# Optimization experiments

Measured on AMD Instinct MI355X. Metric: run time of the kernel, lower is better.

The kernel has to match this reference:

```python
import jax, jax.numpy as jnp
import numpy as np

H = 8        # attention heads
G = 8        # groupnorm groups
EPS = 1e-5

def mish(x):
    return x * jnp.tanh(jnp.logaddexp(x, 0.0))

def conv1d(x, w, b, pad):
    # x: [B,C,L], w: [O,I,K]
    y = jax.lax.conv_general_dilated(x, w, (1,), [(pad, pad)],
                                     dimension_numbers=('NCH', 'OIH', 'NCH'))
    return y + b[None, :, None]

def gn_per_step(x, gamma, beta):
    # torch code reshapes [B,C,L] -> [(B L), C] and applies GroupNorm(G, C):
    # normalize each (b, l) position over channel groups.
    B, C, L = x.shape
    xg = x.reshape(B, G, C // G, L)
    mean = xg.mean(axis=2, keepdims=True)
    var = xg.var(axis=2, keepdims=True)
    xg = (xg - mean) * jax.lax.rsqrt(var + EPS)
    return xg.reshape(B, C, L) * gamma[None, :, None] + beta[None, :, None]

def layernorm(x, g, b):
    mean = x.mean(axis=-1, keepdims=True)
    var = x.var(axis=-1, keepdims=True)
    return (x - mean) * jax.lax.rsqrt(var + EPS) * g + b


def setup_inputs() -> dict:
    key = jax.random.key(0)
    ks = jax.random.split(key, 16)
    B, Cin, Cout, L, N, CD, TD = 64, 256, 512, 512, 77, 768, 512
    w = lambda k, shape, s=0.02: (jax.random.normal(k, shape, jnp.float32) * s)
    return {
        'x': jax.random.normal(ks[0], (B, Cin, L), jnp.float32),
        't': jax.random.normal(ks[1], (B, TD), jnp.float32),
        'cond': jax.random.normal(ks[2], (B, N, CD), jnp.float32),
        'conv0_w': w(ks[3], (Cout, Cin, 5)), 'conv0_b': jnp.zeros((Cout,), jnp.float32),
        'gn0_g': jnp.ones((Cout,), jnp.float32), 'gn0_b': jnp.zeros((Cout,), jnp.float32),
        'tm_w': w(ks[4], (2 * Cout, TD)), 'tm_b': jnp.zeros((2 * Cout,), jnp.float32),
        'conv1_w': w(ks[5], (Cout, Cout, 5)), 'conv1_b': jnp.zeros((Cout,), jnp.float32),
        'gn1_g': jnp.ones((Cout,), jnp.float32), 'gn1_b': jnp.zeros((Cout,), jnp.float32),
        'res_w': w(ks[6], (Cout, Cin, 1)), 'res_b': jnp.zeros((Cout,), jnp.float32),
        'ln_x_g': jnp.ones((Cout,), jnp.float32), 'ln_x_b': jnp.zeros((Cout,), jnp.float32),
        'ln_c_g': jnp.ones((CD,), jnp.float32), 'ln_c_b': jnp.zeros((CD,), jnp.float32),
        'q_w': w(ks[7], (Cout, Cout)), 'q_b': jnp.zeros((Cout,), jnp.float32),
        'k_w': w(ks[8], (Cout, CD)), 'k_b': jnp.zeros((Cout,), jnp.float32),
        'v_w': w(ks[9], (Cout, CD)), 'v_b': jnp.zeros((Cout,), jnp.float32),
        'cond_indices': jnp.arange(B, dtype=jnp.int64 if jax.config.jax_enable_x64 else jnp.int32),
    }


def _forward(x, t, cond,
             conv0_w, conv0_b, gn0_g, gn0_b, tm_w, tm_b,
             conv1_w, conv1_b, gn1_g, gn1_b, res_w, res_b,
             ln_x_g, ln_x_b, ln_c_g, ln_c_b,
             q_w, q_b, k_w, k_b, v_w, v_b, cond_indices):
    Cout = conv0_w.shape[0]
    # ---- ResidualTemporalBlock (adagn=True) ----
    ss = jnp.einsum('bi,oi->bo', mish(t), tm_w) + tm_b        # [B, 2*Cout]
    scale = ss[:, :Cout, None]                                 # chunk dim=1
    shift = ss[:, Cout:, None]
    h = conv1d(x, conv0_w, conv0_b, pad=2)                     # [B,Cout,L]
    h = gn_per_step(h, gn0_g, gn0_b)
    h = mish(h * (1.0 + scale) + shift)                        # ada_shift_scale + Mish
    h = conv1d(h, conv1_w, conv1_b, pad=2)
    h = mish(gn_per_step(h, gn1_g, gn1_b))
    out = h + conv1d(x, res_w, res_b, pad=0)                   # residual 1x1 conv
    # ---- ResidualCrossAttentionLayer (LinearCrossAttention) ----
    xs = out[cond_indices]                                     # [Bc,Cout,L]
    xi = xs.transpose(0, 2, 1)                                 # [Bc,L,Cout]
    cs = cond[cond_indices]                                    # [Bc,N,CD]
    Bc, T, D = xi.shape
    Nn = cs.shape[1]
    Dh = D // H
    q = jnp.einsum('btl,dl->btd', layernorm(xi, ln_x_g, ln_x_b), q_w) + q_b
    cn = layernorm(cs, ln_c_g, ln_c_b)
    k = jnp.einsum('bnl,dl->bnd', cn, k_w) + k_b
    v = jnp.einsum('bnl,dl->bnd', cn, v_w) + v_b
    q = jax.nn.softmax(q.reshape(Bc, T, H, Dh), axis=-1)       # softmax over head dim
    k = jax.nn.softmax(k.reshape(Bc, Nn, H, Dh), axis=1)       # softmax over tokens
    v = v.reshape(Bc, Nn, H, Dh)
    attn = jnp.einsum('bnhd,bnhl->bhdl', k, v)                 # [Bc,H,Dh,Dh] kernel
    y = jnp.einsum('bthd,bhdl->bthl', q, attn).reshape(Bc, T, D)
    return out.at[cond_indices].add(y.transpose(0, 2, 1))


def reference(x, t, cond,
              conv0_w, conv0_b, gn0_g, gn0_b, tm_w, tm_b,
              conv1_w, conv1_b, gn1_g, gn1_b, res_w, res_b,
              ln_x_g, ln_x_b, ln_c_g, ln_c_b,
              q_w, q_b, k_w, k_b, v_w, v_b, cond_indices):
    return _forward(x, t, cond, conv0_w, conv0_b, gn0_g, gn0_b, tm_w, tm_b,
                    conv1_w, conv1_b, gn1_g, gn1_b, res_w, res_b,
                    ln_x_g, ln_x_b, ln_c_g, ln_c_b,
                    q_w, q_b, k_w, k_b, v_w, v_b, cond_indices)
```

## Files before the change

kernel.cpp:

```cpp
#include <hip/hip_runtime.h>
#include <math.h>

#define EPS 1e-5f

typedef __attribute__((ext_vector_type(8))) short short8;
typedef __attribute__((ext_vector_type(4))) float floatx4;

typedef __attribute__((address_space(1))) const void* gas1_t;
typedef __attribute__((address_space(3))) void* las3_t;

__device__ __forceinline__ void glls16(const void* g, void* l) {
    __builtin_amdgcn_global_load_lds((gas1_t)g, (las3_t)l, 16, 0, 0);
}

__device__ __forceinline__ float mishf(float x) {
    float sp = fmaxf(x, 0.0f) + log1pf(expf(-fabsf(x)));
    return x * tanhf(sp);
}
__device__ __forceinline__ unsigned short f2bf(float f) {
    unsigned int u = __float_as_uint(f);
    unsigned int r = (u + 0x7fffu + ((u >> 16) & 1u)) >> 16;
    return (unsigned short)r;
}
__device__ __forceinline__ float bf2f(unsigned short s) {
    return __uint_as_float(((unsigned int)s) << 16);
}
__device__ __forceinline__ unsigned int pk2(unsigned short a, unsigned short b) {
    return (unsigned int)a | ((unsigned int)b << 16);
}

__global__ __launch_bounds__(256) void setup_k(
        const float* __restrict__ conv0_w, const float* __restrict__ conv1_w,
        const float* __restrict__ res_w, const float* __restrict__ q_w,
        const float* __restrict__ k_w, const float* __restrict__ v_w,
        const float* __restrict__ t,
        unsigned short* __restrict__ wp0, unsigned short* __restrict__ wp1,
        unsigned short* __restrict__ wr, unsigned short* __restrict__ wq,
        unsigned short* __restrict__ wk, unsigned short* __restrict__ wvv,
        float* __restrict__ mt,
        unsigned short* __restrict__ xTp, unsigned short* __restrict__ h0Tp) {
    const int blk = blockIdx.x, tid = threadIdx.x;
    if (blk < 2560) {
        int o = blk * 256 + tid;
        int ci = o & 255, co = (o >> 8) & 511, kk = o >> 17;
        wp0[o] = f2bf(conv0_w[((size_t)co * 256 + ci) * 5 + kk]);
    } else if (blk < 7680) {
        int o = (blk - 2560) * 256 + tid;
        int ci = o & 511, co = (o >> 9) & 511, kk = o >> 18;
        wp1[o] = f2bf(conv1_w[((size_t)co * 512 + ci) * 5 + kk]);
    } else if (blk < 7808) {
        int i = (blk - 7680) * 256 + tid;
        float4 f = *(const float4*)&res_w[(size_t)i * 4];
        *(uint2*)&wr[(size_t)i * 4] =
            make_uint2(pk2(f2bf(f.x), f2bf(f.y)), pk2(f2bf(f.z), f2bf(f.w)));
    } else if (blk < 8064) {
        int i = (blk - 7808) * 256 + tid;
        float4 f = *(const float4*)&q_w[(size_t)i * 4];
        *(uint2*)&wq[(size_t)i * 4] =
            make_uint2(pk2(f2bf(f.x), f2bf(f.y)), pk2(f2bf(f.z), f2bf(f.w)));
    } else if (blk < 8448) {
        int i = (blk - 8064) * 256 + tid;
        float4 f = *(const float4*)&k_w[(size_t)i * 4];
        *(uint2*)&wk[(size_t)i * 4] =
            make_uint2(pk2(f2bf(f.x), f2bf(f.y)), pk2(f2bf(f.z), f2bf(f.w)));
    } else if (blk < 8832) {
        int i = (blk - 8448) * 256 + tid;
        float4 f = *(const float4*)&v_w[(size_t)i * 4];
        *(uint2*)&wvv[(size_t)i * 4] =
            make_uint2(pk2(f2bf(f.x), f2bf(f.y)), pk2(f2bf(f.z), f2bf(f.w)));
    } else if (blk < 8960) {
        int i = (blk - 8832) * 256 + tid;
        mt[i] = mishf(t[i]);
    } else if (blk < 8992) {
        int idx = (blk - 8960) * 256 + tid;
        int u = idx * 8;
        int c = u & 255, r4 = (u >> 8) & 3, b = u >> 10;
        int row = (r4 < 2) ? r4 : (512 + r4);
        *(uint4*)&xTp[((size_t)b * 516 + row) * 256 + c] = make_uint4(0, 0, 0, 0);
    } else {
        int idx = (blk - 8992) * 256 + tid;
        int u = idx * 8;
        int c = u & 511, r4 = (u >> 9) & 3, b = u >> 11;
        int row = (r4 < 2) ? r4 : (512 + r4);
        *(uint4*)&h0Tp[((size_t)b * 516 + row) * 512 + c] = make_uint4(0, 0, 0, 0);
    }
}

__global__ __launch_bounds__(256) void xpose_cvt(const float* __restrict__ x,
        unsigned short* __restrict__ xT) {
    __shared__ float tile[64][68];
    const int tid = threadIdx.x;
    const int l0 = blockIdx.x * 64, c0 = blockIdx.y * 64, b = blockIdx.z;
    for (int idx = tid; idx < 64 * 16; idx += 256) {
        int cr = idx >> 4, lc = (idx & 15) * 4;
        float4 f = *(const float4*)&x[((size_t)b * 256 + c0 + cr) * 512 + l0 + lc];
        tile[cr][lc] = f.x; tile[cr][lc + 1] = f.y;
        tile[cr][lc + 2] = f.z; tile[cr][lc + 3] = f.w;
    }
    __syncthreads();
    for (int idx = tid; idx < 64 * 16; idx += 256) {
        int lr = idx >> 4, cc = (idx & 15) * 4;
        *(uint2*)&xT[((size_t)b * 516 + 2 + l0 + lr) * 256 + c0 + cc] =
            make_uint2(pk2(f2bf(tile[cc][lr]), f2bf(tile[cc + 1][lr])),
                       pk2(f2bf(tile[cc + 2][lr]), f2bf(tile[cc + 3][lr])));
    }
}

template<int KD>
__global__ __launch_bounds__(256) void gemm_nt(const float* __restrict__ A,
        const float* __restrict__ W, const float* __restrict__ bias,
        float* __restrict__ C, int M, int N) {
    constexpr int ST = 20;
    __shared__ __align__(16) float As[64 * ST];
    __shared__ __align__(16) float Ws[64 * ST];
    const int tid = threadIdx.x;
    const int r0 = blockIdx.x * 64, c0 = blockIdx.y * 64;
    const int tx = tid & 15, ty = tid >> 4;
    const int lrow = tid >> 2, lk = (tid & 3) * 4;
    float acc[4][4];
#pragma unroll
    for (int i = 0; i < 4; ++i)
#pragma unroll
        for (int j = 0; j < 4; ++j) acc[i][j] = 0.f;
    for (int k0 = 0; k0 < KD; k0 += 16) {
        __syncthreads();
        *(float4*)&As[lrow * ST + lk] =
            *(const float4*)&A[(size_t)(r0 + lrow) * KD + k0 + lk];
        *(float4*)&Ws[lrow * ST + lk] =
            *(const float4*)&W[(size_t)(c0 + lrow) * KD + k0 + lk];
        __syncthreads();
#pragma unroll
        for (int kk = 0; kk < 16; kk += 4) {
            float4 av[4], wv[4];
#pragma unroll
            for (int i = 0; i < 4; ++i)
                av[i] = *(const float4*)&As[(ty + 16 * i) * ST + kk];
#pragma unroll
            for (int j = 0; j < 4; ++j)
                wv[j] = *(const float4*)&Ws[(tx + 16 * j) * ST + kk];
#pragma unroll
            for (int i = 0; i < 4; ++i)
#pragma unroll
                for (int j = 0; j < 4; ++j) {
                    acc[i][j] = fmaf(av[i].x, wv[j].x, acc[i][j]);
                    acc[i][j] = fmaf(av[i].y, wv[j].y, acc[i][j]);
                    acc[i][j] = fmaf(av[i].z, wv[j].z, acc[i][j]);
                    acc[i][j] = fmaf(av[i].w, wv[j].w, acc[i][j]);
                }
        }
    }
#pragma unroll
    for (int j = 0; j < 4; ++j) {
        int c = c0 + tx + 16 * j;
        float bv = bias[c];
#pragma unroll
        for (int i = 0; i < 4; ++i)
            C[(size_t)(r0 + ty + 16 * i) * N + c] = acc[i][j] + bv;
    }
}

template<int CI, bool FILM, bool OPAD>
__global__ __launch_bounds__(256) void conv5_mfma(
        const unsigned short* __restrict__ xb,
        const unsigned short* __restrict__ wp,
        const float* __restrict__ bias,
        const float* __restrict__ gam, const float* __restrict__ bet,
        const float* __restrict__ ss,
        unsigned short* __restrict__ outT) {
    constexpr int NC = CI / 32;
    __shared__ __align__(16) unsigned short xs[2][260 * 32];
    __shared__ __align__(16) unsigned short wsm[2][5 * 64 * 32];
    __shared__ float sgam[64], sbet[64], sbias[64], sscale[64], sshift[64];

    const int tid = threadIdx.x;
    const int l0 = blockIdx.x * 256;
    const int co0 = blockIdx.y * 64;
    const int b = blockIdx.z;
    const int lane = tid & 63;
    const int wv = tid >> 6;
    const int lq = lane & 15, qd = lane >> 4;
    const int wn = wv * 64;

    if (tid < 64) {
        int co = co0 + tid;
        sbias[tid] = bias[co];
        sgam[tid] = gam[co];
        sbet[tid] = bet[co];
        if (FILM) {
            sscale[tid] = ss[(size_t)b * 1024 + co];
            sshift[tid] = ss[(size_t)b * 1024 + 512 + co];
        }
    }

    const unsigned short* gxb = xb + ((size_t)b * 516 + l0) * CI;
    const unsigned short* gwb = wp + (size_t)co0 * CI;

    const unsigned short* xsp[5];
    const unsigned short* wsp[5];
    unsigned sdo[5];
#pragma unroll
    for (int it = 0; it < 5; ++it) {
        int task = it * 256 + tid;
        {
            int ri = task >> 2, pos = task & 3;
            int seg = pos ^ ((ri >> 1) & 3);
            xsp[it] = gxb + (size_t)ri * CI + seg * 8;
        }
        {
            int kk = task >> 8, r = task & 255;
            int col = r >> 2, pos = r & 3;
            int seg = pos ^ ((col >> 1) & 3);
            wsp[it] = gwb + ((size_t)kk * 512 + col) * CI + seg * 8;
        }
        sdo[it] = (unsigned)(it * 256 + wn) * 8;
    }
    const bool xv4 = tid < 16;

    auto stage = [&](int buf) {
#pragma unroll
        for (int it = 0; it < 5; ++it) {
            if (it < 4 || xv4) glls16(xsp[it], &xs[buf][sdo[it]]);
            xsp[it] += 32;
        }
#pragma unroll
        for (int it = 0; it < 5; ++it) {
            glls16(wsp[it], &wsm[buf][sdo[it]]);
            wsp[it] += 32;
        }
    };

    unsigned bvo[5][4], avo[5][4];
#pragma unroll
    for (int kk = 0; kk < 5; ++kk) {
#pragma unroll
        for (int j = 0; j < 4; ++j) {
            int row = wn + j * 16 + lq + kk;
            int pos = qd ^ ((row >> 1) & 3);
            bvo[kk][j] = (unsigned)(row * 32 + pos * 8) * 2u;
        }
#pragma unroll
        for (int i = 0; i < 4; ++i) {
            int crow = i * 16 + lq;
            int pos = qd ^ ((crow >> 1) & 3);
            avo[kk][i] = (unsigned)(kk * 2048 + crow * 32 + pos * 8) * 2u;
        }
    }

    floatx4 acc[4][4];
#pragma unroll
    for (int i = 0; i < 4; ++i)
#pragma unroll
        for (int j = 0; j < 4; ++j) acc[i][j] = (floatx4){0.f, 0.f, 0.f, 0.f};

    auto compute = [&](int buf) {
        const char* xr = (const char*)xs[buf];
        const char* wr_ = (const char*)wsm[buf];
#pragma unroll
        for (int kk = 0; kk < 5; ++kk) {
            short8 bvf[4];
#pragma unroll
            for (int j = 0; j < 4; ++j)
                bvf[j] = *(const short8*)(xr + bvo[kk][j]);
#pragma unroll
            for (int i = 0; i < 4; ++i) {
                short8 av = *(const short8*)(wr_ + avo[kk][i]);
#pragma unroll
                for (int j = 0; j < 4; ++j)
                    acc[i][j] = __builtin_amdgcn_mfma_f32_16x16x32_bf16(
                        av, bvf[j], acc[i][j], 0, 0, 0);
            }
        }
    };

    stage(0);
    stage(1);
    __syncthreads();
#pragma unroll 1
    for (int c = 0; c < NC; ++c) {
        __builtin_amdgcn_s_setprio(1);
        compute(c & 1);
        __builtin_amdgcn_s_setprio(0);
        if (c + 1 < NC) {
            __builtin_amdgcn_s_barrier();
            if (c + 2 < NC) {
                stage(c & 1);
                asm volatile("s_waitcnt vmcnt(9)" ::: "memory");
            } else {
                asm volatile("s_waitcnt vmcnt(0)" ::: "memory");
            }
            __builtin_amdgcn_s_barrier();
        }
    }

    float m_[4], rs_[4];
#pragma unroll
    for (int j = 0; j < 4; ++j) {
        float s1 = 0.f, s2 = 0.f;
#pragma unroll
        for (int i = 0; i < 4; ++i) {
            float4 bv4 = *(const float4*)&sbias[i * 16 + qd * 4];
            float ba[4] = {bv4.x, bv4.y, bv4.z, bv4.w};
#pragma unroll
            for (int r = 0; r < 4; ++r) {
                float v = acc[i][j][r] + ba[r];
                acc[i][j][r] = v;
                s1 += v; s2 += v * v;
            }
        }
        s1 += __shfl_xor(s1, 16, 64); s2 += __shfl_xor(s2, 16, 64);
        s1 += __shfl_xor(s1, 32, 64); s2 += __shfl_xor(s2, 32, 64);
        float mean = s1 * (1.f / 64.f);
        float var = s2 * (1.f / 64.f) - mean * mean;
        m_[j] = mean; rs_[j] = rsqrtf(var + EPS);
    }
#pragma unroll
    for (int j = 0; j < 4; ++j) {
        int l = l0 + wn + j * 16 + lq;
        size_t rowbase = OPAD ? (((size_t)b * 516 + 2 + l) * 512 + co0)
                              : (((size_t)b * 512 + l) * 512 + co0);
#pragma unroll
        for (int i = 0; i < 4; ++i) {
            float4 g4 = *(const float4*)&sgam[i * 16 + qd * 4];
            float4 b4 = *(const float4*)&sbet[i * 16 + qd * 4];
            float ga[4] = {g4.x, g4.y, g4.z, g4.w};
            float be[4] = {b4.x, b4.y, b4.z, b4.w};
            float sa[4] = {0, 0, 0, 0}, sh[4] = {0, 0, 0, 0};
            if (FILM) {
                float4 s4 = *(const float4*)&sscale[i * 16 + qd * 4];
                float4 h4 = *(const float4*)&sshift[i * 16 + qd * 4];
                sa[0] = s4.x; sa[1] = s4.y; sa[2] = s4.z; sa[3] = s4.w;
                sh[0] = h4.x; sh[1] = h4.y; sh[2] = h4.z; sh[3] = h4.w;
            }
            unsigned short o[4];
#pragma unroll
            for (int r = 0; r < 4; ++r) {
                float v = (acc[i][j][r] - m_[j]) * rs_[j] * ga[r] + be[r];
                if (FILM) v = v * (1.f + sa[r]) + sh[r];
                o[r] = f2bf(mishf(v));
            }
            *(uint2*)&outT[rowbase + i * 16 + qd * 4] =
                make_uint2(pk2(o[0], o[1]), pk2(o[2], o[3]));
        }
    }
}

template<int KD, int EPI, bool PADA>
__global__ __launch_bounds__(256) void gemm1_mfma(
        const unsigned short* __restrict__ A,
        const unsigned short* __restrict__ W,
        const float* __restrict__ bias,
        const unsigned short* __restrict__ addT,
        float* __restrict__ outF,
        unsigned short* __restrict__ outB,
        int Mreal) {
    constexpr int NC = KD / 32;
    __shared__ __align__(16) unsigned short xs[2][256 * 32];
    __shared__ __align__(16) unsigned short wsm[2][64 * 32];
    __shared__ float sbias[64];
    const int tid = threadIdx.x;
    const int m0 = blockIdx.x * 256;
    const int n0 = blockIdx.y * 64;
    const int lane = tid & 63;
    const int wv = tid >> 6;
    const int lq = lane & 15, qd = lane >> 4;
    const int wn = wv * 64;
    if (tid < 64) sbias[tid] = bias[n0 + tid];

    const size_t arow0 = PADA ? ((size_t)(m0 >> 9) * 516 + 2 + (m0 & 511))
                              : (size_t)m0;
    const unsigned short* gA = A + arow0 * KD;
    const unsigned short* gW = W + (size_t)n0 * KD;

    const unsigned short* xp[4];
#pragma unroll
    for (int it = 0; it < 4; ++it) {
        int task = it * 256 + tid;
        int ri = task >> 2, pos = task & 3;
        int seg = pos ^ ((ri >> 1) & 3);
        xp[it] = gA + (size_t)ri * KD + seg * 8;
    }
    const unsigned short* wpq;
    {
        int col = tid >> 2, pos = tid & 3;
        int seg = pos ^ ((col >> 1) & 3);
        wpq = gW + (size_t)col * KD + seg * 8;
    }

    auto stage = [&](int buf) {
#pragma unroll
        for (int it = 0; it < 4; ++it) {
            glls16(xp[it], &xs[buf][(unsigned)(it * 256 + wn) * 8]);
            xp[it] += 32;
        }
        glls16(wpq, &wsm[buf][(unsigned)wn * 8]);
        wpq += 32;
    };

    unsigned bvo[4], avo[4];
#pragma unroll
    for (int j = 0; j < 4; ++j) {
        int row = wn + j * 16 + lq;
        int pos = qd ^ ((row >> 1) & 3);
        bvo[j] = (unsigned)(row * 32 + pos * 8) * 2u;
    }
#pragma unroll
    for (int i = 0; i < 4; ++i) {
        int crow = i * 16 + lq;
        int pos = qd ^ ((crow >> 1) & 3);
        avo[i] = (unsigned)(crow * 32 + pos * 8) * 2u;
    }

    floatx4 acc[4][4];
#pragma unroll
    for (int i = 0; i < 4; ++i)
#pragma unroll
        for (int j = 0; j < 4; ++j) acc[i][j] = (floatx4){0.f, 0.f, 0.f, 0.f};

    auto compute = [&](int buf) {
        const char* xr = (const char*)xs[buf];
        const char* wr_ = (const char*)wsm[buf];
        short8 bvf[4];
#pragma unroll
        for (int j = 0; j < 4; ++j)
            bvf[j] = *(const short8*)(xr + bvo[j]);
#pragma unroll
        for (int i = 0; i < 4; ++i) {
            short8 av = *(const short8*)(wr_ + avo[i]);
#pragma unroll
            for (int j = 0; j < 4; ++j)
                acc[i][j] = __builtin_amdgcn_mfma_f32_16x16x32_bf16(
                    av, bvf[j], acc[i][j], 0, 0, 0);
        }
    };

    stage(0);
    stage(1);
    __syncthreads();
#pragma unroll 1
    for (int c = 0; c < NC; ++c) {
        __builtin_amdgcn_s_setprio(1);
        compute(c & 1);
        __builtin_amdgcn_s_setprio(0);
        if (c + 1 < NC) {
            __builtin_amdgcn_s_barrier();
            if (c + 2 < NC) {
                stage(c & 1);
                asm volatile("s_waitcnt vmcnt(5)" ::: "memory");
            } else {
                asm volatile("s_waitcnt vmcnt(0)" ::: "memory");
            }
            __builtin_amdgcn_s_barrier();
        }
    }

#pragma unroll
    for (int i = 0; i < 4; ++i) {
        float4 bv4 = *(const float4*)&sbias[i * 16 + qd * 4];
        float ba[4] = {bv4.x, bv4.y, bv4.z, bv4.w};
#pragma unroll
        for (int j = 0; j < 4; ++j)
#pragma unroll
            for (int r = 0; r < 4; ++r) acc[i][j][r] += ba[r];
    }
    if (EPI == 0) {
#pragma unroll
        for (int j = 0; j < 4; ++j) {
            int m = m0 + wn + j * 16 + lq;
#pragma unroll
            for (int i = 0; i < 4; ++i) {
                int n = n0 + i * 16 + qd * 4;
                uint2 hv = *(const uint2*)&addT[(size_t)m * 512 + n];
                float vr[4];
                vr[0] = acc[i][j][0] + bf2f((unsigned short)(hv.x & 0xffff));
                vr[1] = acc[i][j][1] + bf2f((unsigned short)(hv.x >> 16));
                vr[2] = acc[i][j][2] + bf2f((unsigned short)(hv.y & 0xffff));
                vr[3] = acc[i][j][3] + bf2f((unsigned short)(hv.y >> 16));
                *(uint2*)&outB[(size_t)m * 512 + n] =
                    make_uint2(pk2(f2bf(vr[0]), f2bf(vr[1])),
                               pk2(f2bf(vr[2]), f2bf(vr[3])));
            }
        }
    } else if (EPI == 1) {
#pragma unroll
        for (int j = 0; j < 4; ++j) {
            float mx = -3.4e38f;
#pragma unroll
            for (int i = 0; i < 4; ++i)
#pragma unroll
                for (int r = 0; r < 4; ++r) mx = fmaxf(mx, acc[i][j][r]);
            mx = fmaxf(mx, __shfl_xor(mx, 16, 64));
            mx = fmaxf(mx, __shfl_xor(mx, 32, 64));
            float s = 0.f;
#pragma unroll
            for (int i = 0; i < 4; ++i)
#pragma unroll
                for (int r = 0; r < 4; ++r) {
                    float e = expf(acc[i][j][r] - mx);
                    acc[i][j][r] = e; s += e;
                }
            s += __shfl_xor(s, 16, 64);
            s += __shfl_xor(s, 32, 64);
            float inv = 1.f / s;
            int m = m0 + wn + j * 16 + lq;
#pragma unroll
            for (int i = 0; i < 4; ++i) {
                *(uint2*)&outB[(size_t)m * 512 + n0 + i * 16 + qd * 4] =
                    make_uint2(pk2(f2bf(acc[i][j][0] * inv), f2bf(acc[i][j][1] * inv)),
                               pk2(f2bf(acc[i][j][2] * inv), f2bf(acc[i][j][3] * inv)));
            }
        }
    } else {
#pragma unroll
        for (int j = 0; j < 4; ++j) {
            int m = m0 + wn + j * 16 + lq;
            if (m < Mreal) {
#pragma unroll
                for (int i = 0; i < 4; ++i) {
                    float4 o = {acc[i][j][0], acc[i][j][1], acc[i][j][2], acc[i][j][3]};
                    *(float4*)&outF[(size_t)m * 512 + n0 + i * 16 + qd * 4] = o;
                }
            }
        }
    }
}

__global__ __launch_bounds__(256) void lnrow(const unsigned short* __restrict__ src,
        const float* __restrict__ g, const float* __restrict__ be,
        const int* __restrict__ cidx, unsigned short* __restrict__ dst) {
    const int tid = threadIdx.x;
    const int lane = tid & 63, wv = tid >> 6;
    const int row0 = blockIdx.x * 32 + wv * 8;
    for (int rr = 0; rr < 8; ++rr) {
        int m = row0 + rr;
        int b = m >> 9, t = m & 511;
        int ib = cidx[b];
        const unsigned short* sp = &src[((size_t)ib * 512 + t) * 512 + lane * 8];
        short8 u = *(const short8*)sp;
        float v[8];
        float s1 = 0.f, s2 = 0.f;
#pragma unroll
        for (int k = 0; k < 8; ++k) {
            v[k] = bf2f(((const unsigned short*)&u)[k]);
            s1 += v[k]; s2 += v[k] * v[k];
        }
#pragma unroll
        for (int o = 32; o > 0; o >>= 1) {
            s1 += __shfl_xor(s1, o, 64);
            s2 += __shfl_xor(s2, o, 64);
        }
        float mean = s1 * (1.f / 512.f);
        float var = s2 * (1.f / 512.f) - mean * mean;
        float rs = rsqrtf(var + EPS);
        float4 g0 = *(const float4*)&g[lane * 8];
        float4 g1 = *(const float4*)&g[lane * 8 + 4];
        float4 b0 = *(const float4*)&be[lane * 8];
        float4 b1 = *(const float4*)&be[lane * 8 + 4];
        float ga[8] = {g0.x, g0.y, g0.z, g0.w, g1.x, g1.y, g1.z, g1.w};
        float ba[8] = {b0.x, b0.y, b0.z, b0.w, b1.x, b1.y, b1.z, b1.w};
        unsigned short o8[8];
#pragma unroll
        for (int k = 0; k < 8; ++k)
            o8[k] = f2bf((v[k] - mean) * rs * ga[k] + ba[k]);
        *(uint4*)&dst[(size_t)m * 512 + lane * 8] =
            make_uint4(pk2(o8[0], o8[1]), pk2(o8[2], o8[3]),
                       pk2(o8[4], o8[5]), pk2(o8[6], o8[7]));
    }
}

__global__ __launch_bounds__(256) void lnc_k(const float* __restrict__ cond,
        const float* __restrict__ g, const float* __restrict__ be,
        const int* __restrict__ cidx, unsigned short* __restrict__ cn) {
    const int tid = threadIdx.x;
    const int bn = blockIdx.x;
    const int b = bn / 77, n = bn - b * 77;
    const int ib = cidx[b];
    const float* src = cond + ((size_t)ib * 77 + n) * 768;
    float v[3];
    float s = 0.f, s2 = 0.f;
#pragma unroll
    for (int i = 0; i < 3; ++i) {
        v[i] = src[tid + i * 256];
        s += v[i]; s2 += v[i] * v[i];
    }
#pragma unroll
    for (int o = 32; o > 0; o >>= 1) {
        s += __shfl_xor(s, o, 64);
        s2 += __shfl_xor(s2, o, 64);
    }
    __shared__ float r1[4], r2[4], mv[2];
    if ((tid & 63) == 0) { r1[tid >> 6] = s; r2[tid >> 6] = s2; }
    __syncthreads();
    if (tid == 0) {
        float ts = r1[0] + r1[1] + r1[2] + r1[3];
        float ts2 = r2[0] + r2[1] + r2[2] + r2[3];
        float m = ts * (1.f / 768.f);
        float var = ts2 * (1.f / 768.f) - m * m;
        mv[0] = m; mv[1] = rsqrtf(var + EPS);
    }
    __syncthreads();
    float m = mv[0], rs = mv[1];
    unsigned short* dst = cn + ((size_t)b * 77 + n) * 768;
#pragma unroll
    for (int i = 0; i < 3; ++i) {
        int c = tid + i * 256;
        dst[c] = f2bf((v[i] - m) * rs * g[c] + be[c]);
    }
}

__global__ __launch_bounds__(256) void attn_k(const float* __restrict__ k,
        const float* __restrict__ v, unsigned short* __restrict__ attnT) {
    constexpr int NS = 68;
    __shared__ __align__(16) float ks[77 * NS];
    __shared__ __align__(16) float vs[77 * NS];
    __shared__ float red[2][256];
    const int tid = threadIdx.x;
    const int b = blockIdx.x >> 3, h = blockIdx.x & 7;
    for (int idx = tid; idx < 77 * 16; idx += 256) {
        int n = idx >> 4, dq2 = (idx & 15) * 4;
        *(float4*)&ks[n * NS + dq2] =
            *(const float4*)&k[((size_t)b * 77 + n) * 512 + h * 64 + dq2];
        *(float4*)&vs[n * NS + dq2] =
            *(const float4*)&v[((size_t)b * 77 + n) * 512 + h * 64 + dq2];
    }
    __syncthreads();
    {
        const int d = tid & 63, grp = tid >> 6;
        float mx = -3.4e38f;
        for (int n = grp; n < 77; n += 4) mx = fmaxf(mx, ks[n * NS + d]);
        red[0][grp * 64 + d] = mx;
        __syncthreads();
        mx = fmaxf(fmaxf(red[0][d], red[0][64 + d]),
                   fmaxf(red[0][128 + d], red[0][192 + d]));
        float s = 0.f;
        for (int n = grp; n < 77; n += 4) {
            float e = expf(ks[n * NS + d] - mx);
            ks[n * NS + d] = e; s += e;
        }
        red[1][grp * 64 + d] = s;
        __syncthreads();
        float inv = 1.f / (red[1][d] + red[1][64 + d] + red[1][128 + d] + red[1][192 + d]);
        for (int n = grp; n < 77; n += 4) ks[n * NS + d] *= inv;
    }
    __syncthreads();
    const int e = tid & 63, dq = tid >> 6;
    float acc[16];
#pragma unroll
    for (int u = 0; u < 16; ++u) acc[u] = 0.f;
    for (int n = 0; n < 77; ++n) {
        float vv = vs[n * NS + e];
#pragma unroll
        for (int u4 = 0; u4 < 4; ++u4) {
            float4 kk = *(const float4*)&ks[n * NS + dq * 16 + u4 * 4];
            acc[u4 * 4 + 0] = fmaf(kk.x, vv, acc[u4 * 4 + 0]);
            acc[u4 * 4 + 1] = fmaf(kk.y, vv, acc[u4 * 4 + 1]);
            acc[u4 * 4 + 2] = fmaf(kk.z, vv, acc[u4 * 4 + 2]);
            acc[u4 * 4 + 3] = fmaf(kk.w, vv, acc[u4 * 4 + 3]);
        }
    }
    unsigned short ob[16];
#pragma unroll
    for (int u = 0; u < 16; ++u) ob[u] = f2bf(acc[u]);
    size_t base = (((size_t)b * 8 + h) * 64 + e) * 64 + dq * 16;
    *(uint4*)&attnT[base] = make_uint4(pk2(ob[0], ob[1]), pk2(ob[2], ob[3]),
                                       pk2(ob[4], ob[5]), pk2(ob[6], ob[7]));
    *(uint4*)&attnT[base + 8] = make_uint4(pk2(ob[8], ob[9]), pk2(ob[10], ob[11]),
                                           pk2(ob[12], ob[13]), pk2(ob[14], ob[15]));
}

__global__ __launch_bounds__(256) void yattn_final(
        const unsigned short* __restrict__ q,
        const unsigned short* __restrict__ at,
        const unsigned short* __restrict__ resT,
        const int* __restrict__ cidx, float* __restrict__ out) {
    const int tid = threadIdx.x;
    const int lane = tid & 63, wv = tid >> 6;
    const int lq = lane & 15, qd = lane >> 4;
    const int t0 = blockIdx.x * 256 + wv * 64;
    const int h = blockIdx.y, b = blockIdx.z;
    const int ib = cidx[b];
    floatx4 acc[4][4];
#pragma unroll
    for (int i = 0; i < 4; ++i)
#pragma unroll
        for (int j = 0; j < 4; ++j) acc[i][j] = (floatx4){0.f, 0.f, 0.f, 0.f};
#pragma unroll
    for (int ks = 0; ks < 2; ++ks) {
        short8 av[4], bv[4];
#pragma unroll
        for (int i = 0; i < 4; ++i)
            av[i] = *(const short8*)
                &q[((size_t)(b * 512 + t0 + i * 16 + lq)) * 512 + h * 64 + ks * 32 + qd * 8];
#pragma unroll
        for (int j = 0; j < 4; ++j)
            bv[j] = *(const short8*)
                &at[(((size_t)(b * 8 + h)) * 64 + j * 16 + lq) * 64 + ks * 32 + qd * 8];
#pragma unroll
        for (int i = 0; i < 4; ++i)
#pragma unroll
            for (int j = 0; j < 4; ++j)
                acc[i][j] = __builtin_amdgcn_mfma_f32_16x16x32_bf16(
                    av[i], bv[j], acc[i][j], 0, 0, 0);
    }
#pragma unroll
    for (int j = 0; j < 4; ++j) {
        int c = h * 64 + j * 16 + lq;
#pragma unroll
        for (int i = 0; i < 4; ++i) {
            int tb = t0 + i * 16 + qd * 4;
            float vr[4];
#pragma unroll
            for (int r = 0; r < 4; ++r)
                vr[r] = acc[i][j][r] +
                        bf2f(resT[((size_t)(ib * 512 + tb + r)) * 512 + c]);
            float4 o = {vr[0], vr[1], vr[2], vr[3]};
            *(float4*)&out[((size_t)ib * 512 + c) * 512 + tb] = o;
        }
    }
}

extern "C" void kernel_launch(void* const* d_in, const int* in_sizes, int n_in,
                              void* d_out, int out_size, void* d_ws, size_t ws_size,
                              hipStream_t stream) {
    (void)in_sizes; (void)n_in; (void)out_size; (void)ws_size;
    const float* x       = (const float*)d_in[0];
    const float* t       = (const float*)d_in[1];
    const float* cond    = (const float*)d_in[2];
    const float* conv0_w = (const float*)d_in[3];
    const float* conv0_b = (const float*)d_in[4];
    const float* gn0_g   = (const float*)d_in[5];
    const float* gn0_b   = (const float*)d_in[6];
    const float* tm_w    = (const float*)d_in[7];
    const float* tm_b    = (const float*)d_in[8];
    const float* conv1_w = (const float*)d_in[9];
    const float* conv1_b = (const float*)d_in[10];
    const float* gn1_g   = (const float*)d_in[11];
    const float* gn1_b   = (const float*)d_in[12];
    const float* res_w   = (const float*)d_in[13];
    const float* res_b   = (const float*)d_in[14];
    const float* ln_x_g  = (const float*)d_in[15];
    const float* ln_x_b  = (const float*)d_in[16];
    const float* ln_c_g  = (const float*)d_in[17];
    const float* ln_c_b  = (const float*)d_in[18];
    const float* q_w     = (const float*)d_in[19];
    const float* q_b     = (const float*)d_in[20];
    const float* k_w     = (const float*)d_in[21];
    const float* k_b     = (const float*)d_in[22];
    const float* v_w     = (const float*)d_in[23];
    const float* v_b     = (const float*)d_in[24];
    const int*   cidx    = (const int*)d_in[25];
    float* out = (float*)d_out;

    char* WS = (char*)d_ws;
    unsigned short* xTp   = (unsigned short*)(WS + 0);
    unsigned short* cnb   = (unsigned short*)(WS + 0);
    unsigned short* attnT = (unsigned short*)(WS + 8388608);
    unsigned short* h0Tp  = (unsigned short*)(WS + 16908288);
    unsigned short* xlnT  = (unsigned short*)(WS + 16908288);
    float*          kb    = (float*)(WS + 16908288);
    float*          vb    = (float*)(WS + 27000832);
    unsigned short* h1T   = (unsigned short*)(WS + 50724864);
    unsigned short* qbf   = (unsigned short*)(WS + 50724864);
    unsigned short* outTb = (unsigned short*)(WS + 84279296);
    unsigned short* wp0   = (unsigned short*)(WS + 117833728);
    unsigned short* wp1   = (unsigned short*)(WS + 119144448);
    unsigned short* wr    = (unsigned short*)(WS + 121765888);
    unsigned short* wq    = (unsigned short*)(WS + 122028032);
    unsigned short* wk    = (unsigned short*)(WS + 122552320);
    unsigned short* wvv   = (unsigned short*)(WS + 123338752);
    float*          ssb   = (float*)(WS + 124125184);
    float*          mt    = (float*)(WS + 124387328);

    setup_k<<<dim3(9056), dim3(256), 0, stream>>>(
        conv0_w, conv1_w, res_w, q_w, k_w, v_w, t,
        wp0, wp1, wr, wq, wk, wvv, mt, xTp, h0Tp);
    xpose_cvt<<<dim3(8, 4, 64), dim3(256), 0, stream>>>(x, xTp);
    gemm_nt<512><<<dim3(1, 16), dim3(256), 0, stream>>>(mt, tm_w, tm_b, ssb, 64, 1024);
    conv5_mfma<256, true, true><<<dim3(2, 8, 64), dim3(256), 0, stream>>>(
        xTp, wp0, conv0_b, gn0_g, gn0_b, ssb, h0Tp);
    conv5_mfma<512, false, false><<<dim3(2, 8, 64), dim3(256), 0, stream>>>(
        h0Tp, wp1, conv1_b, gn1_g, gn1_b, (const float*)nullptr, h1T);
    gemm1_mfma<256, 0, true><<<dim3(128, 8), dim3(256), 0, stream>>>(
        xTp, wr, res_b, h1T, (float*)nullptr, outTb, 32768);
    lnrow<<<dim3(1024), dim3(256), 0, stream>>>(outTb, ln_x_g, ln_x_b, cidx, xlnT);
    gemm1_mfma<512, 1, false><<<dim3(128, 8), dim3(256), 0, stream>>>(
        xlnT, wq, q_b, (const unsigned short*)nullptr, (float*)nullptr, qbf, 32768);
    lnc_k<<<dim3(4928), dim3(256), 0, stream>>>(cond, ln_c_g, ln_c_b, cidx, cnb);
    gemm1_mfma<768, 2, false><<<dim3(20, 8), dim3(256), 0, stream>>>(
        cnb, wk, k_b, (const unsigned short*)nullptr, kb, (unsigned short*)nullptr, 4928);
    gemm1_mfma<768, 2, false><<<dim3(20, 8), dim3(256), 0, stream>>>(
        cnb, wvv, v_b, (const unsigned short*)nullptr, vb, (unsigned short*)nullptr, 4928);
    attn_k<<<dim3(512), dim3(256), 0, stream>>>(kb, vb, attnT);
    yattn_final<<<dim3(2, 8, 64), dim3(256), 0, stream>>>(qbf, attnT, outTb, cidx, out);
}
```

Before: 620.9 us.

## Single-buffer weight tiles via register staging to cut LDS and raise occupancy

In the conv5 and gemm1 MFMA kernels, weight tiles are no longer double-buffered in LDS. They are prefetched into registers two chunks ahead and written into a single LDS buffer between barriers. Per-channel bias, gamma, beta and FiLM parameters in conv5 are read straight from global memory instead of being staged in shared memory. Launch bounds now request 3 or 4 blocks per CU. The goal is lower LDS use so more blocks fit per CU, at the cost of extra registers, manual vmcnt bookkeeping and a synchronous LDS store on the critical path each iteration.

```diff
diff --git a/kernel.cpp b/kernel.cpp
--- a/kernel.cpp
+++ b/kernel.cpp
@@ -160,7 +160,7 @@
 }
 
 template<int CI, bool FILM, bool OPAD>
-__global__ __launch_bounds__(256) void conv5_mfma(
+__global__ __launch_bounds__(256, 3) void conv5_mfma(
         const unsigned short* __restrict__ xb,
         const unsigned short* __restrict__ wp,
         const float* __restrict__ bias,
@@ -169,8 +169,7 @@
         unsigned short* __restrict__ outT) {
     constexpr int NC = CI / 32;
     __shared__ __align__(16) unsigned short xs[2][260 * 32];
-    __shared__ __align__(16) unsigned short wsm[2][5 * 64 * 32];
-    __shared__ float sgam[64], sbet[64], sbias[64], sscale[64], sshift[64];
+    __shared__ __align__(16) unsigned short wsm[5 * 64 * 32];
 
     const int tid = threadIdx.x;
     const int l0 = blockIdx.x * 256;
@@ -181,22 +180,11 @@
     const int lq = lane & 15, qd = lane >> 4;
     const int wn = wv * 64;
 
-    if (tid < 64) {
-        int co = co0 + tid;
-        sbias[tid] = bias[co];
-        sgam[tid] = gam[co];
-        sbet[tid] = bet[co];
-        if (FILM) {
-            sscale[tid] = ss[(size_t)b * 1024 + co];
-            sshift[tid] = ss[(size_t)b * 1024 + 512 + co];
-        }
-    }
-
     const unsigned short* gxb = xb + ((size_t)b * 516 + l0) * CI;
     const unsigned short* gwb = wp + (size_t)co0 * CI;
 
     const unsigned short* xsp[5];
-    const unsigned short* wsp[5];
+    const unsigned short* wbp[5];
     unsigned sdo[5];
 #pragma unroll
     for (int it = 0; it < 5; ++it) {
@@ -210,23 +198,30 @@
             int kk = task >> 8, r = task & 255;
             int col = r >> 2, pos = r & 3;
             int seg = pos ^ ((col >> 1) & 3);
-            wsp[it] = gwb + ((size_t)kk * 512 + col) * CI + seg * 8;
+            wbp[it] = gwb + ((size_t)kk * 512 + col) * CI + seg * 8;
         }
         sdo[it] = (unsigned)(it * 256 + wn) * 8;
     }
     const bool xv4 = tid < 16;
 
-    auto stage = [&](int buf) {
+    auto stageX = [&](int buf) {
 #pragma unroll
         for (int it = 0; it < 5; ++it) {
             if (it < 4 || xv4) glls16(xsp[it], &xs[buf][sdo[it]]);
             xsp[it] += 32;
         }
-#pragma unroll
-        for (int it = 0; it < 5; ++it) {
-            glls16(wsp[it], &wsm[buf][sdo[it]]);
-            wsp[it] += 32;
-        }
+    };
+
+    uint4 wreg[5];
+    auto wload = [&](int c) {
+#pragma unroll
+        for (int it = 0; it < 5; ++it)
+            wreg[it] = *(const uint4*)(wbp[it] + (size_t)c * 32);
+    };
+    auto wstore = [&]() {
+#pragma unroll
+        for (int it = 0; it < 5; ++it)
+            *(uint4*)((char*)wsm + (unsigned)(it * 256 + tid) * 16u) = wreg[it];
     };
 
     unsigned bvo[5][4], avo[5][4];
@@ -254,7 +249,7 @@
 
     auto compute = [&](int buf) {
         const char* xr = (const char*)xs[buf];
-        const char* wr_ = (const char*)wsm[buf];
+        const char* wr_ = (const char*)wsm;
 #pragma unroll
         for (int kk = 0; kk < 5; ++kk) {
             short8 bvf[4];
@@ -272,9 +267,13 @@
         }
     };
 
-    stage(0);
-    stage(1);
+    stageX(0);
+#pragma unroll
+    for (int it = 0; it < 5; ++it) glls16(wbp[it], &wsm[sdo[it]]);
+    stageX(1);
+    wload(1);
     __syncthreads();
+
 #pragma unroll 1
     for (int c = 0; c < NC; ++c) {
         __builtin_amdgcn_s_setprio(1);
@@ -282,23 +281,31 @@
         __builtin_amdgcn_s_setprio(0);
         if (c + 1 < NC) {
             __builtin_amdgcn_s_barrier();
+            asm volatile("s_waitcnt vmcnt(9)" ::: "memory");
+            wstore();
             if (c + 2 < NC) {
-                stage(c & 1);
-                asm volatile("s_waitcnt vmcnt(9)" ::: "memory");
+                wload(c + 2);
+                stageX(c & 1);
+                asm volatile("s_waitcnt vmcnt(14)" ::: "memory");
             } else {
                 asm volatile("s_waitcnt vmcnt(0)" ::: "memory");
             }
+            asm volatile("s_waitcnt lgkmcnt(0)" ::: "memory");
             __builtin_amdgcn_s_barrier();
         }
     }
 
+    const float* bb = bias + co0;
+    const float* gb = gam + co0;
+    const float* eb = bet + co0;
+    const float* sb = FILM ? (ss + (size_t)b * 1024 + co0) : nullptr;
     float m_[4], rs_[4];
 #pragma unroll
     for (int j = 0; j < 4; ++j) {
         float s1 = 0.f, s2 = 0.f;
 #pragma unroll
         for (int i = 0; i < 4; ++i) {
-            float4 bv4 = *(const float4*)&sbias[i * 16 + qd * 4];
+            float4 bv4 = *(const float4*)&bb[i * 16 + qd * 4];
             float ba[4] = {bv4.x, bv4.y, bv4.z, bv4.w};
 #pragma unroll
             for (int r = 0; r < 4; ++r) {
@@ -320,14 +327,14 @@
                               : (((size_t)b * 512 + l) * 512 + co0);
 #pragma unroll
         for (int i = 0; i < 4; ++i) {
-            float4 g4 = *(const float4*)&sgam[i * 16 + qd * 4];
-            float4 b4 = *(const float4*)&sbet[i * 16 + qd * 4];
+            float4 g4 = *(const float4*)&gb[i * 16 + qd * 4];
+            float4 b4 = *(const float4*)&eb[i * 16 + qd * 4];
             float ga[4] = {g4.x, g4.y, g4.z, g4.w};
             float be[4] = {b4.x, b4.y, b4.z, b4.w};
             float sa[4] = {0, 0, 0, 0}, sh[4] = {0, 0, 0, 0};
             if (FILM) {
-                float4 s4 = *(const float4*)&sscale[i * 16 + qd * 4];
-                float4 h4 = *(const float4*)&sshift[i * 16 + qd * 4];
+                float4 s4 = *(const float4*)&sb[i * 16 + qd * 4];
+                float4 h4 = *(const float4*)&sb[512 + i * 16 + qd * 4];
                 sa[0] = s4.x; sa[1] = s4.y; sa[2] = s4.z; sa[3] = s4.w;
                 sh[0] = h4.x; sh[1] = h4.y; sh[2] = h4.z; sh[3] = h4.w;
             }
@@ -345,7 +352,7 @@
 }
 
 template<int KD, int EPI, bool PADA>
-__global__ __launch_bounds__(256) void gemm1_mfma(
+__global__ __launch_bounds__(256, 4) void gemm1_mfma(
         const unsigned short* __restrict__ A,
         const unsigned short* __restrict__ W,
         const float* __restrict__ bias,
@@ -355,7 +362,7 @@
         int Mreal) {
     constexpr int NC = KD / 32;
     __shared__ __align__(16) unsigned short xs[2][256 * 32];
-    __shared__ __align__(16) unsigned short wsm[2][64 * 32];
+    __shared__ __align__(16) unsigned short wsm[64 * 32];
     __shared__ float sbias[64];
     const int tid = threadIdx.x;
     const int m0 = blockIdx.x * 256;
@@ -379,21 +386,25 @@
         int seg = pos ^ ((ri >> 1) & 3);
         xp[it] = gA + (size_t)ri * KD + seg * 8;
     }
-    const unsigned short* wpq;
+    const unsigned short* wbp;
     {
         int col = tid >> 2, pos = tid & 3;
         int seg = pos ^ ((col >> 1) & 3);
-        wpq = gW + (size_t)col * KD + seg * 8;
-    }
-
-    auto stage = [&](int buf) {
+        wbp = gW + (size_t)col * KD + seg * 8;
+    }
+
+    auto stageX = [&](int buf) {
 #pragma unroll
         for (int it = 0; it < 4; ++it) {
             glls16(xp[it], &xs[buf][(unsigned)(it * 256 + wn) * 8]);
             xp[it] += 32;
         }
-        glls16(wpq, &wsm[buf][(unsigned)wn * 8]);
-        wpq += 32;
+    };
+
+    uint4 wreg;
+    auto wload = [&](int c) { wreg = *(const uint4*)(wbp + (size_t)c * 32); };
+    auto wstore = [&]() {
+        *(uint4*)((char*)wsm + (unsigned)tid * 16u) = wreg;
     };
 
     unsigned bvo[4], avo[4];
@@ -418,7 +429,7 @@
 
     auto compute = [&](int buf) {
         const char* xr = (const char*)xs[buf];
-        const char* wr_ = (const char*)wsm[buf];
+        const char* wr_ = (const char*)wsm;
         short8 bvf[4];
 #pragma unroll
         for (int j = 0; j < 4; ++j)
@@ -433,9 +444,14 @@
         }
     };
 
-    stage(0);
-    stage(1);
+    stageX(0);
+    {
+        glls16(wbp, &wsm[(unsigned)wn * 8]);
+    }
+    stageX(1);
+    wload(1);
     __syncthreads();
+
 #pragma unroll 1
     for (int c = 0; c < NC; ++c) {
         __builtin_amdgcn_s_setprio(1);
@@ -443,12 +459,16 @@
         __builtin_amdgcn_s_setprio(0);
         if (c + 1 < NC) {
             __builtin_amdgcn_s_barrier();
+            asm volatile("s_waitcnt vmcnt(4)" ::: "memory");
+            wstore();
             if (c + 2 < NC) {
-                stage(c & 1);
+                wload(c + 2);
+                stageX(c & 1);
                 asm volatile("s_waitcnt vmcnt(5)" ::: "memory");
             } else {
                 asm volatile("s_waitcnt vmcnt(0)" ::: "memory");
             }
+            asm volatile("s_waitcnt lgkmcnt(0)" ::: "memory");
             __builtin_amdgcn_s_barrier();
         }
     }
```

New measurement: 1.051 ms. +69.3%, slower.
